# Kernel optimization log

Measured on AMD Instinct MI355X. Metric: run time of the kernel, lower is better.

## Reference

```python
import jax, jax.numpy as jnp
import numpy as np

B, S, INPUT_DIM = 16, 2048, 768
G, V = 2, 320            # num_codebooks, codebook_size
D = INPUT_DIM // G       # codebook_dim = 384
OUT_DIM = 768
TEMP = 1.0
EPS = 1e-10


def setup_inputs() -> dict:
    key = jax.random.key(0)
    ks = jax.random.split(key, 7)
    z = jax.random.normal(ks[0], (B, S, INPUT_DIM), dtype=jnp.float32)
    noise = jax.random.uniform(ks[1], (B, S, G, V), dtype=jnp.float32)
    # logits_projection: Linear(codebook_dim -> codebook_size)
    W_logits = jax.random.normal(ks[2], (D, V), dtype=jnp.float32) / np.sqrt(D)
    b_logits = jnp.zeros((V,), dtype=jnp.float32)
    codebooks = jax.random.normal(ks[3], (G, V, D), dtype=jnp.float32)
    # output_projection: Linear(input_dim -> output_dim)
    W_out = jax.random.normal(ks[4], (INPUT_DIM, OUT_DIM), dtype=jnp.float32) / np.sqrt(INPUT_DIM)
    b_out = jnp.zeros((OUT_DIM,), dtype=jnp.float32)
    return {"z": z, "noise": noise, "W_logits": W_logits, "b_logits": b_logits,
            "codebooks": codebooks, "W_out": W_out, "b_out": b_out}


def reference(z, noise, W_logits, b_logits, codebooks, W_out, b_out):
    b, s, _ = z.shape
    g, v, d = codebooks.shape
    zr = z.reshape(b, s, g, d)                                   # [B,S,G,D]
    logits = jnp.einsum('bsgd,dv->bsgv', zr, W_logits) + b_logits
    # training-mode gumbel noise
    gumbel = -jnp.log(-jnp.log(noise + EPS) + EPS)
    logits = (logits + gumbel) / TEMP
    probs = jax.nn.softmax(logits, axis=-1)                      # [B,S,G,V]
    indices = jnp.argmax(probs, axis=-1)                         # [B,S,G]
    hard = jax.nn.one_hot(indices, v, dtype=probs.dtype)
    quantized = hard - jax.lax.stop_gradient(probs) + probs      # straight-through
    quantized = jnp.einsum('bsgv,gvd->bsgd', quantized, codebooks)
    quantized = quantized.reshape(b, s, g * d)
    return quantized @ W_out + b_out
```

## Files before the change

### kernel.cpp

```cpp
#include <hip/hip_runtime.h>
#include <math.h>

#define BS_TOT 32768
#define IN_DIM 768
#define G_N 2
#define V_N 320
#define D_N 384
#define OUT_N 768
#define EPS_F 1e-10f

typedef _Float16 f16x8 __attribute__((ext_vector_type(8)));
typedef float    f32x16 __attribute__((ext_vector_type(16)));

#define GLOBAL_LOAD_LDS16(gaddr, laddr)                                        \
  __builtin_amdgcn_global_load_lds(                                            \
      (const __attribute__((address_space(1))) unsigned int*)(gaddr),          \
      (__attribute__((address_space(3))) unsigned int*)(laddr), 16, 0, 0)

__global__ __launch_bounds__(256) void prep_w(
    const float* __restrict__ Wl, _Float16* __restrict__ Wp)
{
    int e = blockIdx.x * 256 + threadIdx.x;
    if (e >= D_N * V_N) return;
    int k = e / V_N, v = e - k * V_N;
    int kt = k >> 5, kl = k & 31, kh = kl >> 3, j = kl & 7;
    float w = Wl[e];
    _Float16 a = (_Float16)w;
    float r = (w - (float)a) * 4096.f;
    Wp[((size_t)((kt * 2 + 0) * 4 + kh) * V_N + v) * 8 + j] = a;
    Wp[((size_t)((kt * 2 + 1) * 4 + kh) * V_N + v) * 8 + j] = (_Float16)r;
}

__global__ __launch_bounds__(256) void precompute_P(
    const float* __restrict__ cb, const float* __restrict__ Wo,
    float* __restrict__ P)
{
    const int tid = threadIdx.x;
    const int c0  = blockIdx.x * 256;
    const int r0  = blockIdx.y * 8;
    const int g   = r0 / V_N;
    __shared__ float As[8][D_N];
    {
        const float4* src = (const float4*)(cb + (size_t)r0 * D_N);
        float4* dst = (float4*)(&As[0][0]);
        #pragma unroll
        for (int p = 0; p < 3; ++p) dst[tid + p * 256] = src[tid + p * 256];
    }
    __syncthreads();
    float acc[8];
    #pragma unroll
    for (int i = 0; i < 8; ++i) acc[i] = 0.f;
    const float* wp = Wo + ((size_t)g * D_N) * OUT_N + c0 + tid;
    for (int d = 0; d < D_N; d += 4) {
        float w0 = wp[(size_t)(d + 0) * OUT_N];
        float w1 = wp[(size_t)(d + 1) * OUT_N];
        float w2 = wp[(size_t)(d + 2) * OUT_N];
        float w3 = wp[(size_t)(d + 3) * OUT_N];
        #pragma unroll
        for (int i = 0; i < 8; ++i) {
            float4 a = *(const float4*)&As[i][d];
            acc[i] = fmaf(a.x, w0, acc[i]);
            acc[i] = fmaf(a.y, w1, acc[i]);
            acc[i] = fmaf(a.z, w2, acc[i]);
            acc[i] = fmaf(a.w, w3, acc[i]);
        }
    }
    #pragma unroll
    for (int i = 0; i < 8; ++i)
        P[(size_t)(r0 + i) * OUT_N + c0 + tid] = acc[i];
}

__global__ __launch_bounds__(256, 2) void logits_mfma(
    const float* __restrict__ z, const float* __restrict__ noise,
    const f16x8* __restrict__ Wp, const float* __restrict__ bl,
    int* __restrict__ idx)
{
    const int tid  = threadIdx.x;
    const int g    = blockIdx.y;
    const int m0   = blockIdx.x * 64;
    const int ln   = tid & 63;
    const int wv   = tid >> 6;
    const int wrow = wv >> 1;
    const int wcol = wv & 1;
    const int lh   = ln >> 5;
    const int l5   = ln & 31;

    __shared__ f16x8 BsV[2560];
    __shared__ f16x8 AsV[512];
    __shared__ float sVal[2][64];
    __shared__ int   sIdx[2][64];

    f32x16 accM[5], accC[5];
    #pragma unroll
    for (int nf = 0; nf < 5; ++nf)
        #pragma unroll
        for (int i = 0; i < 16; ++i) { accM[nf][i] = 0.f; accC[nf][i] = 0.f; }

    const int arow_s = tid & 63;
    const int akh    = tid >> 6;
    const float* zrow = z + (size_t)(m0 + arow_s) * IN_DIM + g * D_N + akh * 8;

    float4 ap0 = *(const float4*)(zrow);
    float4 ap1 = *(const float4*)(zrow + 4);

    const int arow = wrow * 32 + l5;
    const int bcol = wcol * 160 + l5;

    for (int kt = 0; kt < 12; ++kt) {
        __syncthreads();
        #pragma unroll
        for (int p = 0; p < 10; ++p) {
            GLOBAL_LOAD_LDS16(Wp + (size_t)kt * 2560 + wv * 640 + p * 64 + ln,
                              BsV + wv * 640 + p * 64);
        }
        {
            float x[8] = {ap0.x, ap0.y, ap0.z, ap0.w, ap1.x, ap1.y, ap1.z, ap1.w};
            f16x8 h1, h2;
            #pragma unroll
            for (int i = 0; i < 8; ++i) {
                _Float16 a = (_Float16)x[i];
                float r = (x[i] - (float)a) * 4096.f;
                h1[i] = a;
                h2[i] = (_Float16)r;
            }
            AsV[(0 * 4 + akh) * 64 + arow_s] = h1;
            AsV[(1 * 4 + akh) * 64 + arow_s] = h2;
        }
        __syncthreads();
        if (kt < 11) {
            ap0 = *(const float4*)(zrow + (kt + 1) * 32);
            ap1 = *(const float4*)(zrow + (kt + 1) * 32 + 4);
        }
        #pragma unroll
        for (int b = 0; b < 2; ++b) {
            f16x8 a0 = AsV[(0 * 4 + b * 2 + lh) * 64 + arow];
            f16x8 a1 = AsV[(1 * 4 + b * 2 + lh) * 64 + arow];
            #pragma unroll
            for (int nf = 0; nf < 5; ++nf) {
                f16x8 b0 = BsV[(0 * 4 + b * 2 + lh) * 320 + bcol + nf * 32];
                f16x8 b1 = BsV[(1 * 4 + b * 2 + lh) * 320 + bcol + nf * 32];
                accM[nf] = __builtin_amdgcn_mfma_f32_32x32x16_f16(a0, b0, accM[nf], 0, 0, 0);
                accC[nf] = __builtin_amdgcn_mfma_f32_32x32x16_f16(a0, b1, accC[nf], 0, 0, 0);
                accC[nf] = __builtin_amdgcn_mfma_f32_32x32x16_f16(a1, b0, accC[nf], 0, 0, 0);
            }
        }
    }

    float blv[5];
    #pragma unroll
    for (int nf = 0; nf < 5; ++nf) blv[nf] = bl[wcol * 160 + nf * 32 + l5];

    #pragma unroll
    for (int r = 0; r < 16; ++r) {
        const int rowloc = (r & 3) + 8 * (r >> 2) + 4 * lh;
        const int grow   = m0 + wrow * 32 + rowloc;
        const float* np_ = noise + ((size_t)grow * G_N + g) * V_N + wcol * 160 + l5;
        float best = -INFINITY; int bi = 0;
        #pragma unroll
        for (int nf = 0; nf < 5; ++nf) {
            float u   = np_[nf * 32];
            float gum = -__logf(-__logf(u + EPS_F) + EPS_F);
            float v   = accM[nf][r] + 2.44140625e-4f * accC[nf][r] + blv[nf] + gum;
            int   c   = wcol * 160 + nf * 32 + l5;
            if (v > best) { best = v; bi = c; }
        }
        #pragma unroll
        for (int off = 1; off < 32; off <<= 1) {
            float ov = __shfl_xor(best, off);
            int   oi = __shfl_xor(bi, off);
            if (ov > best || (ov == best && oi < bi)) { best = ov; bi = oi; }
        }
        if (l5 == 0) {
            sVal[wcol][wrow * 32 + rowloc] = best;
            sIdx[wcol][wrow * 32 + rowloc] = bi;
        }
    }
    __syncthreads();
    if (tid < 64) {
        float v0 = sVal[0][tid], v1 = sVal[1][tid];
        int   i0 = sIdx[0][tid], i1 = sIdx[1][tid];
        int   b  = (v1 > v0 || (v1 == v0 && i1 < i0)) ? i1 : i0;
        idx[(size_t)(m0 + tid) * G_N + g] = b;
    }
}

__global__ __launch_bounds__(256) void gather_out(
    const float* __restrict__ P, const int* __restrict__ idx,
    const float* __restrict__ bo, float* __restrict__ out)
{
    const int tid  = threadIdx.x;
    const int row0 = blockIdx.x << 2;
    #pragma unroll
    for (int p = 0; p < 3; ++p) {
        int f   = tid + (p << 8);
        int rl  = f / 192;
        int c4  = f - rl * 192;
        int row = row0 + rl;
        int i0  = idx[row * 2];
        int i1  = idx[row * 2 + 1];
        float4 a  = ((const float4*)(P + (size_t)i0 * OUT_N))[c4];
        float4 b2 = ((const float4*)(P + (size_t)(V_N + i1) * OUT_N))[c4];
        float4 c  = ((const float4*)bo)[c4];
        float4 r;
        r.x = a.x + b2.x + c.x;
        r.y = a.y + b2.y + c.y;
        r.z = a.z + b2.z + c.z;
        r.w = a.w + b2.w + c.w;
        ((float4*)(out + (size_t)row * OUT_N))[c4] = r;
    }
}

extern "C" void kernel_launch(void* const* d_in, const int* in_sizes, int n_in,
                              void* d_out, int out_size, void* d_ws, size_t ws_size,
                              hipStream_t stream)
{
    const float* z     = (const float*)d_in[0];
    const float* noise = (const float*)d_in[1];
    const float* Wl    = (const float*)d_in[2];
    const float* bl    = (const float*)d_in[3];
    const float* cb    = (const float*)d_in[4];
    const float* Wo    = (const float*)d_in[5];
    const float* bo    = (const float*)d_in[6];
    float* out = (float*)d_out;

    float*     P   = (float*)d_ws;
    int*       idx = (int*)((char*)d_ws + 1966080);
    _Float16*  Wp  = (_Float16*)((char*)d_ws + 2228224);

    prep_w<<<(D_N * V_N + 255) / 256, 256, 0, stream>>>(Wl, Wp);

    dim3 gA(OUT_N / 256, (G_N * V_N) / 8);
    precompute_P<<<gA, 256, 0, stream>>>(cb, Wo, P);

    dim3 gB(BS_TOT / 64, G_N);
    logits_mfma<<<gB, 256, 0, stream>>>(z, noise, (const f16x8*)Wp, bl, idx);

    gather_out<<<BS_TOT / 4, 256, 0, stream>>>(P, idx, bo, out);
}
```

Measured before the change: 338.5 us.

## Double-buffer logits GEMM with 128-row tiles and 16-wide K steps

The logits MFMA kernel now handles 128 rows per block, with each wave computing two 32-row M fragments so every B fragment loaded from LDS is reused twice. The K loop uses 16-element steps with double-buffered A and B tiles in LDS, so the next tile's global-to-LDS load overlaps the current MFMAs and one barrier per iteration is enough. prep_w repacks W to match the new K-step layout. This doubles accumulator registers (occupancy bound lowered to 1 block) and halves the grid, which risks lower occupancy and fewer blocks to hide latency.

```diff
diff --git a/kernel.cpp b/kernel.cpp
--- a/kernel.cpp
+++ b/kernel.cpp
@@ -23,12 +23,12 @@
     int e = blockIdx.x * 256 + threadIdx.x;
     if (e >= D_N * V_N) return;
     int k = e / V_N, v = e - k * V_N;
-    int kt = k >> 5, kl = k & 31, kh = kl >> 3, j = kl & 7;
+    int kt2 = k >> 4, kh = (k >> 3) & 1, j = k & 7;
     float w = Wl[e];
     _Float16 a = (_Float16)w;
     float r = (w - (float)a) * 4096.f;
-    Wp[((size_t)((kt * 2 + 0) * 4 + kh) * V_N + v) * 8 + j] = a;
-    Wp[((size_t)((kt * 2 + 1) * 4 + kh) * V_N + v) * 8 + j] = (_Float16)r;
+    Wp[((size_t)(((kt2 * 2 + 0) * 2 + kh) * V_N) + v) * 8 + j] = a;
+    Wp[((size_t)(((kt2 * 2 + 1) * 2 + kh) * V_N) + v) * 8 + j] = (_Float16)r;
 }
 
 __global__ __launch_bounds__(256) void precompute_P(
@@ -70,14 +70,14 @@
         P[(size_t)(r0 + i) * OUT_N + c0 + tid] = acc[i];
 }
 
-__global__ __launch_bounds__(256, 2) void logits_mfma(
+__global__ __launch_bounds__(256, 1) void logits_mfma(
     const float* __restrict__ z, const float* __restrict__ noise,
     const f16x8* __restrict__ Wp, const float* __restrict__ bl,
     int* __restrict__ idx)
 {
     const int tid  = threadIdx.x;
     const int g    = blockIdx.y;
-    const int m0   = blockIdx.x * 64;
+    const int m0   = blockIdx.x * 128;
     const int ln   = tid & 63;
     const int wv   = tid >> 6;
     const int wrow = wv >> 1;
@@ -85,98 +85,125 @@
     const int lh   = ln >> 5;
     const int l5   = ln & 31;
 
-    __shared__ f16x8 BsV[2560];
-    __shared__ f16x8 AsV[512];
-    __shared__ float sVal[2][64];
-    __shared__ int   sIdx[2][64];
-
-    f32x16 accM[5], accC[5];
-    #pragma unroll
-    for (int nf = 0; nf < 5; ++nf)
-        #pragma unroll
-        for (int i = 0; i < 16; ++i) { accM[nf][i] = 0.f; accC[nf][i] = 0.f; }
-
-    const int arow_s = tid & 63;
-    const int akh    = tid >> 6;
-    const float* zrow = z + (size_t)(m0 + arow_s) * IN_DIM + g * D_N + akh * 8;
-
-    float4 ap0 = *(const float4*)(zrow);
-    float4 ap1 = *(const float4*)(zrow + 4);
-
-    const int arow = wrow * 32 + l5;
-    const int bcol = wcol * 160 + l5;
-
-    for (int kt = 0; kt < 12; ++kt) {
-        __syncthreads();
-        #pragma unroll
-        for (int p = 0; p < 10; ++p) {
-            GLOBAL_LOAD_LDS16(Wp + (size_t)kt * 2560 + wv * 640 + p * 64 + ln,
-                              BsV + wv * 640 + p * 64);
-        }
-        {
-            float x[8] = {ap0.x, ap0.y, ap0.z, ap0.w, ap1.x, ap1.y, ap1.z, ap1.w};
+    __shared__ f16x8 Bs[2][1280];
+    __shared__ f16x8 As[2][512];
+    __shared__ float sVal[2][128];
+    __shared__ int   sIdx[2][128];
+
+    f32x16 accM[2][5], accC[2][5];
+    #pragma unroll
+    for (int mf = 0; mf < 2; ++mf)
+        #pragma unroll
+        for (int nf = 0; nf < 5; ++nf)
+            #pragma unroll
+            for (int i = 0; i < 16; ++i) { accM[mf][nf][i] = 0.f; accC[mf][nf][i] = 0.f; }
+
+    const int ar = tid & 127;
+    const int ah = tid >> 7;
+    const float* zrow = z + (size_t)(m0 + ar) * IN_DIM + g * D_N + ah * 8;
+
+    #pragma unroll
+    for (int q = 0; q < 5; ++q)
+        GLOBAL_LOAD_LDS16(Wp + wv * 320 + q * 64 + ln, &Bs[0][wv * 320 + q * 64]);
+    {
+        float4 c0 = *(const float4*)zrow;
+        float4 c1 = *(const float4*)(zrow + 4);
+        float x[8] = {c0.x, c0.y, c0.z, c0.w, c1.x, c1.y, c1.z, c1.w};
+        f16x8 h1, h2;
+        #pragma unroll
+        for (int i = 0; i < 8; ++i) {
+            _Float16 a = (_Float16)x[i];
+            h1[i] = a;
+            h2[i] = (_Float16)((x[i] - (float)a) * 4096.f);
+        }
+        As[0][(0 + ah) * 128 + ar] = h1;
+        As[0][(2 + ah) * 128 + ar] = h2;
+    }
+    float4 n0 = *(const float4*)(zrow + 16);
+    float4 n1 = *(const float4*)(zrow + 20);
+    __syncthreads();
+
+    const int arow0 = wrow * 64 + l5;
+    const int bc    = wcol * 160 + l5;
+
+    for (int kt = 0; kt < 24; ++kt) {
+        const int p = kt & 1;
+        if (kt < 23) {
+            #pragma unroll
+            for (int q = 0; q < 5; ++q)
+                GLOBAL_LOAD_LDS16(Wp + (size_t)(kt + 1) * 1280 + wv * 320 + q * 64 + ln,
+                                  &Bs[1 - p][wv * 320 + q * 64]);
+            float x[8] = {n0.x, n0.y, n0.z, n0.w, n1.x, n1.y, n1.z, n1.w};
             f16x8 h1, h2;
             #pragma unroll
             for (int i = 0; i < 8; ++i) {
                 _Float16 a = (_Float16)x[i];
-                float r = (x[i] - (float)a) * 4096.f;
                 h1[i] = a;
-                h2[i] = (_Float16)r;
-            }
-            AsV[(0 * 4 + akh) * 64 + arow_s] = h1;
-            AsV[(1 * 4 + akh) * 64 + arow_s] = h2;
+                h2[i] = (_Float16)((x[i] - (float)a) * 4096.f);
+            }
+            As[1 - p][(0 + ah) * 128 + ar] = h1;
+            As[1 - p][(2 + ah) * 128 + ar] = h2;
+        }
+        if (kt < 22) {
+            n0 = *(const float4*)(zrow + (kt + 2) * 16);
+            n1 = *(const float4*)(zrow + (kt + 2) * 16 + 4);
+        }
+        {
+            f16x8 a00 = As[p][(0 + lh) * 128 + arow0];
+            f16x8 a01 = As[p][(2 + lh) * 128 + arow0];
+            f16x8 a10 = As[p][(0 + lh) * 128 + arow0 + 32];
+            f16x8 a11 = As[p][(2 + lh) * 128 + arow0 + 32];
+            #pragma unroll
+            for (int nf = 0; nf < 5; ++nf) {
+                f16x8 b0 = Bs[p][(0 + lh) * 320 + bc + nf * 32];
+                f16x8 b1 = Bs[p][(2 + lh) * 320 + bc + nf * 32];
+                accM[0][nf] = __builtin_amdgcn_mfma_f32_32x32x16_f16(a00, b0, accM[0][nf], 0, 0, 0);
+                accC[0][nf] = __builtin_amdgcn_mfma_f32_32x32x16_f16(a00, b1, accC[0][nf], 0, 0, 0);
+                accC[0][nf] = __builtin_amdgcn_mfma_f32_32x32x16_f16(a01, b0, accC[0][nf], 0, 0, 0);
+                accM[1][nf] = __builtin_amdgcn_mfma_f32_32x32x16_f16(a10, b0, accM[1][nf], 0, 0, 0);
+                accC[1][nf] = __builtin_amdgcn_mfma_f32_32x32x16_f16(a10, b1, accC[1][nf], 0, 0, 0);
+                accC[1][nf] = __builtin_amdgcn_mfma_f32_32x32x16_f16(a11, b0, accC[1][nf], 0, 0, 0);
+            }
         }
         __syncthreads();
-        if (kt < 11) {
-            ap0 = *(const float4*)(zrow + (kt + 1) * 32);
-            ap1 = *(const float4*)(zrow + (kt + 1) * 32 + 4);
-        }
-        #pragma unroll
-        for (int b = 0; b < 2; ++b) {
-            f16x8 a0 = AsV[(0 * 4 + b * 2 + lh) * 64 + arow];
-            f16x8 a1 = AsV[(1 * 4 + b * 2 + lh) * 64 + arow];
+    }
+
+    float blv[5];
+    #pragma unroll
+    for (int nf = 0; nf < 5; ++nf) blv[nf] = bl[wcol * 160 + nf * 32 + l5];
+
+    #pragma unroll
+    for (int mf = 0; mf < 2; ++mf) {
+        #pragma unroll
+        for (int r = 0; r < 16; ++r) {
+            const int rowloc = (r & 3) + 8 * (r >> 2) + 4 * lh;
+            const int growb  = wrow * 64 + mf * 32 + rowloc;
+            const int grow   = m0 + growb;
+            const float* nrow = noise + ((size_t)grow * G_N + g) * V_N + wcol * 160 + l5;
+            float best = -INFINITY; int bi = 0;
             #pragma unroll
             for (int nf = 0; nf < 5; ++nf) {
-                f16x8 b0 = BsV[(0 * 4 + b * 2 + lh) * 320 + bcol + nf * 32];
-                f16x8 b1 = BsV[(1 * 4 + b * 2 + lh) * 320 + bcol + nf * 32];
-                accM[nf] = __builtin_amdgcn_mfma_f32_32x32x16_f16(a0, b0, accM[nf], 0, 0, 0);
-                accC[nf] = __builtin_amdgcn_mfma_f32_32x32x16_f16(a0, b1, accC[nf], 0, 0, 0);
-                accC[nf] = __builtin_amdgcn_mfma_f32_32x32x16_f16(a1, b0, accC[nf], 0, 0, 0);
-            }
-        }
-    }
-
-    float blv[5];
-    #pragma unroll
-    for (int nf = 0; nf < 5; ++nf) blv[nf] = bl[wcol * 160 + nf * 32 + l5];
-
-    #pragma unroll
-    for (int r = 0; r < 16; ++r) {
-        const int rowloc = (r & 3) + 8 * (r >> 2) + 4 * lh;
-        const int grow   = m0 + wrow * 32 + rowloc;
-        const float* np_ = noise + ((size_t)grow * G_N + g) * V_N + wcol * 160 + l5;
-        float best = -INFINITY; int bi = 0;
-        #pragma unroll
-        for (int nf = 0; nf < 5; ++nf) {
-            float u   = np_[nf * 32];
-            float gum = -__logf(-__logf(u + EPS_F) + EPS_F);
-            float v   = accM[nf][r] + 2.44140625e-4f * accC[nf][r] + blv[nf] + gum;
-            int   c   = wcol * 160 + nf * 32 + l5;
-            if (v > best) { best = v; bi = c; }
-        }
-        #pragma unroll
-        for (int off = 1; off < 32; off <<= 1) {
-            float ov = __shfl_xor(best, off);
-            int   oi = __shfl_xor(bi, off);
-            if (ov > best || (ov == best && oi < bi)) { best = ov; bi = oi; }
-        }
-        if (l5 == 0) {
-            sVal[wcol][wrow * 32 + rowloc] = best;
-            sIdx[wcol][wrow * 32 + rowloc] = bi;
+                float u   = nrow[nf * 32];
+                float gum = -__logf(-__logf(u + EPS_F) + EPS_F);
+                float v   = accM[mf][nf][r] + 2.44140625e-4f * accC[mf][nf][r]
+                            + blv[nf] + gum;
+                int   c   = wcol * 160 + nf * 32 + l5;
+                if (v > best) { best = v; bi = c; }
+            }
+            #pragma unroll
+            for (int off = 1; off < 32; off <<= 1) {
+                float ov = __shfl_xor(best, off);
+                int   oi = __shfl_xor(bi, off);
+                if (ov > best || (ov == best && oi < bi)) { best = ov; bi = oi; }
+            }
+            if (l5 == 0) {
+                sVal[wcol][growb] = best;
+                sIdx[wcol][growb] = bi;
+            }
         }
     }
     __syncthreads();
-    if (tid < 64) {
+    if (tid < 128) {
         float v0 = sVal[0][tid], v1 = sVal[1][tid];
         int   i0 = sIdx[0][tid], i1 = sIdx[1][tid];
         int   b  = (v1 > v0 || (v1 == v0 && i1 < i0)) ? i1 : i0;
@@ -232,7 +259,7 @@
     dim3 gA(OUT_N / 256, (G_N * V_N) / 8);
     precompute_P<<<gA, 256, 0, stream>>>(cb, Wo, P);
 
-    dim3 gB(BS_TOT / 64, G_N);
+    dim3 gB(BS_TOT / 128, G_N);
     logits_mfma<<<gB, 256, 0, stream>>>(z, noise, (const f16x8*)Wp, bl, idx);
 
     gather_out<<<BS_TOT / 4, 256, 0, stream>>>(P, idx, bo, out);
```

Measured after the change: 592.7 us. 1.75x slower.
